# Kernel tuning notes

Hardware: AMD Instinct MI355X
Metric: run time of the kernel (lower is better)

## Reference

```python
import jax, jax.numpy as jnp
import numpy as np

MARGIN = 0.2  # init kwarg
_EPS = 1e-12


def _pairwise_dist(x):
    # Euclidean cdist via the Gram trick; safe sqrt so grads stay finite at d=0.
    sq = jnp.sum(x * x, axis=1)
    d2 = sq[:, None] + sq[None, :] - 2.0 * (x @ x.T)
    d2 = jnp.maximum(d2, 0.0)
    safe = jnp.where(d2 > _EPS, d2, _EPS)
    return jnp.where(d2 > _EPS, jnp.sqrt(safe), 0.0)


def setup_inputs() -> dict:
    key = jax.random.key(0)
    k1, k2 = jax.random.split(key)
    B, D = 8192, 128
    embeddings = jax.random.normal(k1, (B, D), dtype=jnp.float32)
    labels = jax.random.randint(k2, (B,), 0, 64)
    return {"embeddings": embeddings, "labels": labels}


def reference(embeddings, labels):
    B = embeddings.shape[0]
    d = _pairwise_dist(embeddings)                      # [B, B]
    eq = labels[None, :] == labels[:, None]             # [B, B] bool (incl. diag)
    pos_mask = eq.astype(d.dtype) - jnp.eye(B, dtype=d.dtype)  # positives, no self
    hardest_positive = jnp.max(d * pos_mask, axis=1)    # [B]
    max_dist = jnp.max(d)
    # push non-negatives (same label, incl. self) out of the min
    hardest_negative = jnp.min(d + max_dist * eq.astype(d.dtype), axis=1)  # [B]
    losses = jax.nn.relu(hardest_positive - hardest_negative + MARGIN)
    return jnp.mean(losses)
```

## Files before the change

### kernel.cpp

```cpp
#include <hip/hip_runtime.h>
#include <hip/hip_bf16.h>


#define BB 8192
#define DD 128
#define MARGIN 0.2f
#define EPS 1e-12f

#define COLS_PER_BLOCK 512
#define ROWS_PER_BLOCK 128
#define STAGE_COLS 64
#define NSTAGES (COLS_PER_BLOCK / STAGE_COLS)
#define STAGE_SHORTS (STAGE_COLS * DD)

typedef __attribute__((ext_vector_type(8))) short short8;
typedef __attribute__((ext_vector_type(16))) float f32x16;

__device__ inline unsigned short f2bf(float f) {
    __hip_bfloat16 h = __float2bfloat16(f);
    unsigned short u;
    __builtin_memcpy(&u, &h, 2);
    return u;
}

__global__ __launch_bounds__(256) void prep_kernel(
    const float* __restrict__ x, const int* __restrict__ lab,
    unsigned short* __restrict__ xb, float2* __restrict__ meta,
    unsigned* __restrict__ hp2, unsigned* __restrict__ mn2) {
    int t = blockIdx.x * blockDim.x + threadIdx.x;
    int row = t >> 5;
    const float4 v = reinterpret_cast<const float4*>(x)[t];

    union { unsigned short u[4]; uint2 w; } p;
    p.u[0] = f2bf(v.x); p.u[1] = f2bf(v.y);
    p.u[2] = f2bf(v.z); p.u[3] = f2bf(v.w);
    reinterpret_cast<uint2*>(xb)[t] = p.w;

    float s = v.x * v.x + v.y * v.y + v.z * v.z + v.w * v.w;
    #pragma unroll
    for (int m = 16; m >= 1; m >>= 1) s += __shfl_xor(s, m, 64);
    if ((t & 31) == 0) meta[row] = make_float2(s, __int_as_float(lab[row]));

    if (t < BB) { hp2[t] = 0u; mn2[t] = 0x7f800000u; }
}

__global__ __launch_bounds__(256, 4) void triplet_main(
    const unsigned short* __restrict__ xb, const float2* __restrict__ meta,
    unsigned* __restrict__ hp2, unsigned* __restrict__ mn2) {
    const int tid  = threadIdx.x;
    const int wave = tid >> 6;
    const int lane = tid & 63;
    const int l31  = lane & 31;
    const int lh1  = lane >> 5;
    const int rbase = blockIdx.x * ROWS_PER_BLOCK + wave * 32;
    const int cbase = blockIdx.y * COLS_PER_BLOCK;

    __shared__ unsigned short sb[2][STAGE_SHORTS];
    __shared__ float2 smeta[COLS_PER_BLOCK];

    short8 a[8];
    {
        const unsigned short* ar = xb + (size_t)(rbase + l31) * DD + lh1 * 8;
        #pragma unroll
        for (int s = 0; s < 8; ++s)
            a[s] = *reinterpret_cast<const short8*>(ar + s * 16);
    }

    unsigned li4[4];
    float hp[16], mn[16];
    #pragma unroll
    for (int q = 0; q < 4; ++q) {
        unsigned w = 0;
        #pragma unroll
        for (int k = 0; k < 4; ++k) {
            const int rl = 8 * q + 4 * lh1 + k;
            w |= ((unsigned)__float_as_int(meta[rbase + rl].y) & 255u) << (8 * k);
        }
        li4[q] = w;
    }
    #pragma unroll
    for (int r = 0; r < 16; ++r) { hp[r] = -__builtin_inff(); mn[r] = __builtin_inff(); }

    smeta[tid] = meta[cbase + tid];
    smeta[tid + 256] = meta[cbase + tid + 256];

    auto stage = [&](int g, int buf) {
        const char* src_base = (const char*)(xb + (size_t)(cbase + g * STAGE_COLS) * DD);
        #pragma unroll
        for (int p = 0; p < 4; ++p) {
            const int o   = p * 4096 + tid * 16;
            const int row = o >> 8;
            const int byt = (o & 255) ^ ((row & 7) << 4);
            const char* src = src_base + row * 256 + byt;
            char* dst = (char*)&sb[buf][0] + p * 4096 + wave * 1024;
            __builtin_amdgcn_global_load_lds(
                (const __attribute__((address_space(1))) void*)src,
                (__attribute__((address_space(3))) void*)dst, 16, 0, 0);
        }
    };

    auto compute_group = [&](int st, int gg, int buf) {
        const char* base = (const char*)&sb[buf][0];
        const int jl = gg * 32 + l31;
        const int rowoff = jl * 256;
        const int swz = (jl & 7) << 4;
        f32x16 acc = {};
        short8 b[4];
        #pragma unroll
        for (int s = 0; s < 4; ++s)
            b[s] = *reinterpret_cast<const short8*>(
                base + rowoff + ((s * 32 + lh1 * 16) ^ swz));
        #pragma unroll
        for (int s = 0; s < 4; ++s)
            acc = __builtin_amdgcn_mfma_f32_32x32x16_bf16(a[s], b[s], acc, 0, 0, 0);
        #pragma unroll
        for (int s = 0; s < 4; ++s)
            b[s] = *reinterpret_cast<const short8*>(
                base + rowoff + (((s + 4) * 32 + lh1 * 16) ^ swz));
        #pragma unroll
        for (int s = 0; s < 4; ++s)
            acc = __builtin_amdgcn_mfma_f32_32x32x16_bf16(a[s + 4], b[s], acc, 0, 0, 0);

        const float2 mj = smeta[st * STAGE_COLS + jl];
        const float sqj = mj.x;
        const int   lj  = __float_as_int(mj.y);
        #pragma unroll
        for (int q = 0; q < 4; ++q) {
            const unsigned lw = li4[q];
            #pragma unroll
            for (int k = 0; k < 4; ++k) {
                const int r = q * 4 + k;
                const float d2p = fmaf(acc[r], -2.0f, sqj);
                const bool eq = (int)((lw >> (8 * k)) & 255u) == lj;
                hp[r] = fmaxf(hp[r], eq ? d2p : -__builtin_inff());
                mn[r] = fminf(mn[r], eq ? __builtin_inff() : d2p);
            }
        }
    };

    stage(0, 0);
    asm volatile("s_waitcnt vmcnt(0)" ::: "memory");
    __syncthreads();
    for (int st = 0; st < NSTAGES; ++st) {
        if (st + 1 < NSTAGES) stage(st + 1, (st + 1) & 1);
        compute_group(st, 0, st & 1);
        compute_group(st, 1, st & 1);
        asm volatile("s_waitcnt vmcnt(0)" ::: "memory");
        __syncthreads();
    }

    #pragma unroll
    for (int r = 0; r < 16; ++r) {
        const int rl = (r & 3) + 8 * (r >> 2) + 4 * lh1;
        const float sqi = meta[rbase + rl].x;
        hp[r] = fmaxf(sqi + hp[r], 0.0f);
        mn[r] = sqi + mn[r];
    }
    #pragma unroll
    for (int m = 1; m < 32; m <<= 1) {
        #pragma unroll
        for (int r = 0; r < 16; ++r) {
            hp[r] = fmaxf(hp[r], __shfl_xor(hp[r], m, 64));
            mn[r] = fminf(mn[r], __shfl_xor(mn[r], m, 64));
        }
    }
    if (l31 == 0) {
        #pragma unroll
        for (int r = 0; r < 16; ++r) {
            const int i = rbase + (r & 3) + 8 * (r >> 2) + 4 * lh1;
            atomicMax(&hp2[i], __float_as_uint(hp[r]));
            atomicMin(&mn2[i], __float_as_uint(mn[r]));
        }
    }
}

__device__ inline float d_of(float d2) {
    return (d2 > EPS) ? sqrtf(d2) : 0.0f;
}

__global__ __launch_bounds__(1024) void finalize_kernel(
    const uint4* __restrict__ hp2v, const uint4* __restrict__ mn2v,
    float* __restrict__ out) {
    float acc = 0.0f;
    #pragma unroll
    for (int it = 0; it < 2; ++it) {
        const int i = it * 1024 + threadIdx.x;
        const uint4 h = hp2v[i];
        const uint4 m = mn2v[i];
        const unsigned hu[4] = {h.x, h.y, h.z, h.w};
        const unsigned mu[4] = {m.x, m.y, m.z, m.w};
        #pragma unroll
        for (int k = 0; k < 4; ++k) {
            const float hpv = d_of(__uint_as_float(hu[k]));
            const float mnv = d_of(__uint_as_float(mu[k]));
            acc += fmaxf(hpv - mnv + MARGIN, 0.0f);
        }
    }
    #pragma unroll
    for (int m = 1; m < 64; m <<= 1) acc += __shfl_xor(acc, m, 64);
    __shared__ float ws[16];
    const int wave = threadIdx.x >> 6;
    if ((threadIdx.x & 63) == 0) ws[wave] = acc;
    __syncthreads();
    if (threadIdx.x == 0) {
        float s = 0.0f;
        #pragma unroll
        for (int w = 0; w < 16; ++w) s += ws[w];
        out[0] = s / (float)BB;
    }
}

extern "C" void kernel_launch(void* const* d_in, const int* in_sizes, int n_in,
                              void* d_out, int out_size, void* d_ws, size_t ws_size,
                              hipStream_t stream) {
    const float* x = (const float*)d_in[0];
    const int* lab = (const int*)d_in[1];
    float* out = (float*)d_out;

    char* ws = (char*)d_ws;
    unsigned short* xb = (unsigned short*)ws;
    float2* meta = (float2*)(ws + (size_t)BB * DD * 2);
    unsigned* hp2 = (unsigned*)(ws + (size_t)BB * DD * 2 + BB * 8);
    unsigned* mn2 = (unsigned*)(ws + (size_t)BB * DD * 2 + BB * 12);

    prep_kernel<<<(BB * DD / 4) / 256, 256, 0, stream>>>(x, lab, xb, meta, hp2, mn2);
    dim3 grid(BB / ROWS_PER_BLOCK, BB / COLS_PER_BLOCK);
    triplet_main<<<grid, 256, 0, stream>>>(xb, meta, hp2, mn2);
    finalize_kernel<<<1, 1024, 0, stream>>>((const uint4*)hp2, (const uint4*)mn2, out);
}
```

Measured before the change: 49.99 us.

## Double rows per block, add triple-buffered staging, parallelize finalize

Each block now runs 512 threads covering 256 rows, so every staged column tile is reused across twice as many rows. The LDS pipeline moves from double to triple buffering with partial vmcnt waits, keeping two stages in flight, and the swizzle widens to 16 rows. The single-block finalize becomes an 8-block reduction that sums into a 64-bit fixed-point accumulator, with a last-block-done counter writing the result. The trade-offs are fewer, larger blocks with more LDS each, which may lower occupancy, and extra atomic work in finalize.

```diff
diff --git a/kernel.cpp b/kernel.cpp
--- a/kernel.cpp
+++ b/kernel.cpp
@@ -8,9 +8,9 @@
 #define EPS 1e-12f
 
 #define COLS_PER_BLOCK 512
-#define ROWS_PER_BLOCK 128
+#define ROWS_PER_BLOCK 256
 #define STAGE_COLS 64
-#define NSTAGES (COLS_PER_BLOCK / STAGE_COLS)
+#define NSTAGES 8
 #define STAGE_SHORTS (STAGE_COLS * DD)
 
 typedef __attribute__((ext_vector_type(8))) short short8;
@@ -26,7 +26,8 @@
 __global__ __launch_bounds__(256) void prep_kernel(
     const float* __restrict__ x, const int* __restrict__ lab,
     unsigned short* __restrict__ xb, float2* __restrict__ meta,
-    unsigned* __restrict__ hp2, unsigned* __restrict__ mn2) {
+    unsigned* __restrict__ hp2, unsigned* __restrict__ mn2,
+    unsigned long long* __restrict__ fsum, unsigned* __restrict__ fdone) {
     int t = blockIdx.x * blockDim.x + threadIdx.x;
     int row = t >> 5;
     const float4 v = reinterpret_cast<const float4*>(x)[t];
@@ -42,9 +43,10 @@
     if ((t & 31) == 0) meta[row] = make_float2(s, __int_as_float(lab[row]));
 
     if (t < BB) { hp2[t] = 0u; mn2[t] = 0x7f800000u; }
-}
-
-__global__ __launch_bounds__(256, 4) void triplet_main(
+    if (t == 0) { *fsum = 0ull; *fdone = 0u; }
+}
+
+__global__ __launch_bounds__(512, 4) void triplet_main(
     const unsigned short* __restrict__ xb, const float2* __restrict__ meta,
     unsigned* __restrict__ hp2, unsigned* __restrict__ mn2) {
     const int tid  = threadIdx.x;
@@ -55,7 +57,7 @@
     const int rbase = blockIdx.x * ROWS_PER_BLOCK + wave * 32;
     const int cbase = blockIdx.y * COLS_PER_BLOCK;
 
-    __shared__ unsigned short sb[2][STAGE_SHORTS];
+    __shared__ unsigned short sb[3][STAGE_SHORTS];
     __shared__ float2 smeta[COLS_PER_BLOCK];
 
     short8 a[8];
@@ -82,17 +84,16 @@
     for (int r = 0; r < 16; ++r) { hp[r] = -__builtin_inff(); mn[r] = __builtin_inff(); }
 
     smeta[tid] = meta[cbase + tid];
-    smeta[tid + 256] = meta[cbase + tid + 256];
 
     auto stage = [&](int g, int buf) {
         const char* src_base = (const char*)(xb + (size_t)(cbase + g * STAGE_COLS) * DD);
         #pragma unroll
-        for (int p = 0; p < 4; ++p) {
-            const int o   = p * 4096 + tid * 16;
+        for (int p = 0; p < 2; ++p) {
+            const int o   = p * 8192 + tid * 16;
             const int row = o >> 8;
-            const int byt = (o & 255) ^ ((row & 7) << 4);
+            const int byt = (o & 255) ^ ((row & 15) << 4);
             const char* src = src_base + row * 256 + byt;
-            char* dst = (char*)&sb[buf][0] + p * 4096 + wave * 1024;
+            char* dst = (char*)&sb[buf][0] + p * 8192 + wave * 1024;
             __builtin_amdgcn_global_load_lds(
                 (const __attribute__((address_space(1))) void*)src,
                 (__attribute__((address_space(3))) void*)dst, 16, 0, 0);
@@ -103,7 +104,7 @@
         const char* base = (const char*)&sb[buf][0];
         const int jl = gg * 32 + l31;
         const int rowoff = jl * 256;
-        const int swz = (jl & 7) << 4;
+        const int swz = (jl & 15) << 4;
         f32x16 acc = {};
         short8 b[4];
         #pragma unroll
@@ -139,15 +140,22 @@
     };
 
     stage(0, 0);
-    asm volatile("s_waitcnt vmcnt(0)" ::: "memory");
-    __syncthreads();
-    for (int st = 0; st < NSTAGES; ++st) {
-        if (st + 1 < NSTAGES) stage(st + 1, (st + 1) & 1);
-        compute_group(st, 0, st & 1);
-        compute_group(st, 1, st & 1);
-        asm volatile("s_waitcnt vmcnt(0)" ::: "memory");
-        __syncthreads();
-    }
+    stage(1, 1);
+    #define PIPE_ITER(ST, PEND)                                            \
+        asm volatile("s_waitcnt vmcnt(" #PEND ")" ::: "memory");           \
+        __syncthreads();                                                   \
+        if ((ST) + 2 < NSTAGES) stage((ST) + 2, ((ST) + 2) % 3);           \
+        compute_group((ST), 0, (ST) % 3);                                  \
+        compute_group((ST), 1, (ST) % 3);
+    PIPE_ITER(0, 2)
+    PIPE_ITER(1, 2)
+    PIPE_ITER(2, 2)
+    PIPE_ITER(3, 2)
+    PIPE_ITER(4, 2)
+    PIPE_ITER(5, 2)
+    PIPE_ITER(6, 2)
+    PIPE_ITER(7, 0)
+    #undef PIPE_ITER
 
     #pragma unroll
     for (int r = 0; r < 16; ++r) {
@@ -179,23 +187,14 @@
 }
 
 __global__ __launch_bounds__(1024) void finalize_kernel(
-    const uint4* __restrict__ hp2v, const uint4* __restrict__ mn2v,
+    const unsigned* __restrict__ hp2, const unsigned* __restrict__ mn2,
+    unsigned long long* __restrict__ fsum, unsigned* __restrict__ fdone,
     float* __restrict__ out) {
-    float acc = 0.0f;
-    #pragma unroll
-    for (int it = 0; it < 2; ++it) {
-        const int i = it * 1024 + threadIdx.x;
-        const uint4 h = hp2v[i];
-        const uint4 m = mn2v[i];
-        const unsigned hu[4] = {h.x, h.y, h.z, h.w};
-        const unsigned mu[4] = {m.x, m.y, m.z, m.w};
-        #pragma unroll
-        for (int k = 0; k < 4; ++k) {
-            const float hpv = d_of(__uint_as_float(hu[k]));
-            const float mnv = d_of(__uint_as_float(mu[k]));
-            acc += fmaxf(hpv - mnv + MARGIN, 0.0f);
-        }
-    }
+    const int i = blockIdx.x * 1024 + threadIdx.x;
+    const float hpv = d_of(__uint_as_float(hp2[i]));
+    const float mnv = d_of(__uint_as_float(mn2[i]));
+    float acc = fmaxf(hpv - mnv + MARGIN, 0.0f);
+
     #pragma unroll
     for (int m = 1; m < 64; m <<= 1) acc += __shfl_xor(acc, m, 64);
     __shared__ float ws[16];
@@ -206,7 +205,13 @@
         float s = 0.0f;
         #pragma unroll
         for (int w = 0; w < 16; ++w) s += ws[w];
-        out[0] = s / (float)BB;
+        atomicAdd(fsum, (unsigned long long)((double)s * 4294967296.0));
+        __threadfence();
+        const unsigned old = atomicAdd(fdone, 1u);
+        if (old == gridDim.x - 1) {
+            const unsigned long long total = atomicAdd(fsum, 0ull);
+            out[0] = (float)((double)total / 4294967296.0 / (double)BB);
+        }
     }
 }
 
@@ -222,9 +227,11 @@
     float2* meta = (float2*)(ws + (size_t)BB * DD * 2);
     unsigned* hp2 = (unsigned*)(ws + (size_t)BB * DD * 2 + BB * 8);
     unsigned* mn2 = (unsigned*)(ws + (size_t)BB * DD * 2 + BB * 12);
-
-    prep_kernel<<<(BB * DD / 4) / 256, 256, 0, stream>>>(x, lab, xb, meta, hp2, mn2);
+    unsigned long long* fsum = (unsigned long long*)(ws + (size_t)BB * DD * 2 + BB * 16);
+    unsigned* fdone = (unsigned*)(ws + (size_t)BB * DD * 2 + BB * 16 + 8);
+
+    prep_kernel<<<(BB * DD / 4) / 256, 256, 0, stream>>>(x, lab, xb, meta, hp2, mn2, fsum, fdone);
     dim3 grid(BB / ROWS_PER_BLOCK, BB / COLS_PER_BLOCK);
-    triplet_main<<<grid, 256, 0, stream>>>(xb, meta, hp2, mn2);
-    finalize_kernel<<<1, 1024, 0, stream>>>((const uint4*)hp2, (const uint4*)mn2, out);
-}
+    triplet_main<<<grid, 512, 0, stream>>>(xb, meta, hp2, mn2);
+    finalize_kernel<<<BB / 1024, 1024, 0, stream>>>(hp2, mn2, fsum, fdone, out);
+}
```

Result: slower. 152.5 us (+205.0%).
